# Optimization experiments

Hardware: AMD Instinct MI355X
Metric: run time of the kernel (lower is better)

## Reference

```python
import jax, jax.numpy as jnp
import numpy as np

GROUPS = 32
EPS = 1e-5


def group_norm(x, gamma, beta):
    # x: [B, C, H, W]; normalize over (C//G, H, W) within each of G groups
    B, C, H, W = x.shape
    xg = x.reshape(B, GROUPS, C // GROUPS, H, W)
    mean = xg.mean(axis=(2, 3, 4), keepdims=True)
    var = xg.var(axis=(2, 3, 4), keepdims=True)
    xg = (xg - mean) * jax.lax.rsqrt(var + EPS)
    x = xg.reshape(B, C, H, W)
    return x * gamma[None, :, None, None] + beta[None, :, None, None]


def conv1x1(x, W, b):
    # 1x1 conv == pointwise linear over channels. x: [B,C,H,W], W: [Cout,Cin]
    return jnp.einsum('oc,bchw->bohw', W, x) + b[None, :, None, None]


def setup_inputs() -> dict:
    key = jax.random.key(0)
    ks = jax.random.split(key, 6)
    B, C, H, W = 16, 512, 32, 32
    scale = 1.0 / np.sqrt(C)  # ~kaiming-ish init for 1x1 convs
    return {
        'x': jax.random.normal(ks[0], (B, C, H, W), jnp.float32),
        'gn_gamma': jnp.ones((C,), jnp.float32),
        'gn_beta': jnp.zeros((C,), jnp.float32),
        'Wq': jax.random.normal(ks[1], (C, C), jnp.float32) * scale,
        'bq': jnp.zeros((C,), jnp.float32),
        'Wk': jax.random.normal(ks[2], (C, C), jnp.float32) * scale,
        'bk': jnp.zeros((C,), jnp.float32),
        'Wv': jax.random.normal(ks[3], (C, C), jnp.float32) * scale,
        'bv': jnp.zeros((C,), jnp.float32),
        'Wp': jax.random.normal(ks[4], (C, C), jnp.float32) * scale,
        'bp': jnp.zeros((C,), jnp.float32),
    }


def reference(x, gn_gamma, gn_beta, Wq, bq, Wk, bk, Wv, bv, Wp, bp):
    B, C, H, W = x.shape
    h = group_norm(x, gn_gamma, gn_beta)
    q = conv1x1(h, Wq, bq).reshape(B, C, H * W)  # [B,C,T]
    k = conv1x1(h, Wk, bk).reshape(B, C, H * W)
    v = conv1x1(h, Wv, bv).reshape(B, C, H * W)
    # scores [B, T(query), S(key)] = q^T k, scaled by C^{-1/2}
    w = jnp.einsum('bct,bcs->bts', q, k) * (C ** -0.5)
    w = jax.nn.softmax(w, axis=-1)
    h = jnp.einsum('bts,bcs->bct', w, v).reshape(B, C, H, W)
    h = conv1x1(h, Wp, bp)
    return x + h
```

## Files before the change

### kernel.cpp

```cpp
#include <hip/hip_runtime.h>

typedef unsigned short u16;
typedef __bf16 bf16x8 __attribute__((ext_vector_type(8)));
typedef float f32x4 __attribute__((ext_vector_type(4)));

__device__ __forceinline__ u16 f2bf(float f) {
    unsigned u = __builtin_bit_cast(unsigned, f);
    u += 0x7fffu + ((u >> 16) & 1u);
    return (u16)(u >> 16);
}

#define GLDS16(g, l) __builtin_amdgcn_global_load_lds( \
    (const __attribute__((address_space(1))) void*)(g), \
    (__attribute__((address_space(3))) void*)(l), 16, 0, 0)

#define QK_SCALE 0.044194173824159216f

__global__ __launch_bounds__(256) void convert_kernel(
    const float* __restrict__ Wq, const float* __restrict__ Wk,
    const float* __restrict__ Wv, const float* __restrict__ Wp,
    const float* __restrict__ bq, const float* __restrict__ bk,
    const float* __restrict__ bv,
    u16* __restrict__ Wqkv, u16* __restrict__ Wpb, float* __restrict__ bqkv,
    float* __restrict__ rsum)
{
    int idx = blockIdx.x * 256 + threadIdx.x;
    if (idx < 786432) {
        int which = idx >> 18;
        int off   = idx & 262143;
        if (which == 0)
            Wqkv[idx] = f2bf(Wq[off] * QK_SCALE);
        else
            Wqkv[idx] = f2bf(((which == 1) ? Wk : Wv)[off]);
    } else {
        int off = idx - 786432;
        Wpb[off] = f2bf(Wp[off]);
    }
    if (idx < 1536) {
        float bvv = (idx < 512) ? bq[idx] * QK_SCALE
                  : (idx < 1024) ? bk[idx & 511] : bv[idx & 511];
        bqkv[idx] = bvv;
    }
    if (idx < 16384) rsum[idx] = 0.f;
}

__global__ __launch_bounds__(256) void gn_stats(
    const float* __restrict__ x, float2* __restrict__ stats)
{
    const int g = blockIdx.x, b = blockIdx.y, tid = threadIdx.x;
    const float* xg = x + ((size_t)b * 512 + (size_t)g * 16) * 1024;

    float s = 0.f, s2 = 0.f;
    const float4* x4 = (const float4*)xg;
    #pragma unroll 4
    for (int i = tid; i < 4096; i += 256) {
        float4 v = x4[i];
        s  += v.x + v.y + v.z + v.w;
        s2 += v.x * v.x + v.y * v.y + v.z * v.z + v.w * v.w;
    }
    #pragma unroll
    for (int off = 32; off; off >>= 1) {
        s  += __shfl_down(s, off);
        s2 += __shfl_down(s2, off);
    }
    __shared__ float rs[4], rs2[4];
    const int w = tid >> 6;
    if ((tid & 63) == 0) { rs[w] = s; rs2[w] = s2; }
    __syncthreads();
    if (tid == 0) {
        float S  = rs[0] + rs[1] + rs[2] + rs[3];
        float S2 = rs2[0] + rs2[1] + rs2[2] + rs2[3];
        float mean = S * (1.f / 16384.f);
        float var  = S2 * (1.f / 16384.f) - mean * mean;
        stats[b * 32 + g] = make_float2(mean, rsqrtf(var + 1e-5f));
    }
}

__global__ __launch_bounds__(256) void gn_apply(
    const float* __restrict__ x, const float* __restrict__ gamma,
    const float* __restrict__ beta, const float2* __restrict__ stats,
    u16* __restrict__ ht)
{
    const int tc = blockIdx.x, b = blockIdx.y, tid = threadIdx.x;
    const int t0 = tc * 32;

    __shared__ float2 st[32];
    __shared__ float ga[512], be[512];
    __shared__ __align__(16) u16 tile[512 * 32];

    if (tid < 32) st[tid] = stats[b * 32 + tid];
    for (int c = tid; c < 512; c += 256) { ga[c] = gamma[c]; be[c] = beta[c]; }
    __syncthreads();

    #pragma unroll
    for (int pass = 0; pass < 16; pass++) {
        const int c = pass * 32 + (tid >> 3);
        const int f = tid & 7;
        float4 v = *(const float4*)(x + ((size_t)(b * 512 + c)) * 1024 + t0 + f * 4);
        float2 s = st[c >> 4];
        float sc = s.y * ga[c];
        float sh = be[c] - s.x * sc;
        ushort4 hv = {f2bf(v.x * sc + sh), f2bf(v.y * sc + sh),
                      f2bf(v.z * sc + sh), f2bf(v.w * sc + sh)};
        const int slot = f ^ (c & 7) ^ ((c >> 3) & 7);
        *(ushort4*)(tile + c * 32 + slot * 4) = hv;
    }
    __syncthreads();

    #pragma unroll
    for (int p = 0; p < 8; p++) {
        const int t = p * 4 + (tid >> 6);
        const int l = tid & 63;
        u16 tmp[8];
        #pragma unroll
        for (int e = 0; e < 8; e++) {
            const int c = l * 8 + e;
            const int slot = (t >> 2) ^ (c & 7) ^ ((c >> 3) & 7);
            tmp[e] = tile[c * 32 + slot * 4 + (t & 3)];
        }
        *(uint4*)(ht + ((size_t)b * 1024 + t0 + t) * 512 + l * 8) = *(uint4*)tmp;
    }
}

template <int MODE>
__global__ __launch_bounds__(512, 2) void gemm_nt(
    const u16* __restrict__ A, const u16* __restrict__ B,
    size_t strideA, size_t strideB, int lda, int ldb, int K,
    u16* __restrict__ o0, u16* __restrict__ o1, u16* __restrict__ o2,
    float* __restrict__ fo, const float* __restrict__ bias,
    const float* __restrict__ xres)
{
    __shared__ __align__(16) u16 smem[73728];
    u16* As = smem;
    u16* Bs = smem + 49152;

    const int tid  = threadIdx.x;
    const int lane = tid & 63;
    const int wave = tid >> 6;
    const int wm   = (wave & 3) * 64;
    const int wn   = (wave >> 2) * 64;

    const int gx = gridDim.x, gy = gridDim.y;
    int f = blockIdx.x + gx * (blockIdx.y + gy * blockIdx.z);
    const int nwg = gx * gy * (int)gridDim.z;
    f = (f & 7) * (nwg >> 3) + (f >> 3);
    const int bx  = f % gx;
    const int byz = f / gx;
    const int by  = byz % gy;
    const int b   = byz / gy;

    const u16* Ab = A + (size_t)b * strideA + (size_t)by * 256 * lda;
    const u16* Bb = B + (size_t)b * strideB + (size_t)bx * 128 * ldb;

    const int srow = tid >> 3;
    const int sc   = tid & 7;
    const int scg  = sc ^ (srow & 7);

    const u16* aSrc[4]; int aDst[4];
    #pragma unroll
    for (int u = 0; u < 4; u++) {
        aSrc[u] = Ab + (size_t)(u * 64 + srow) * lda + scg * 8;
        aDst[u] = (u * 64 + srow) * 64 + sc * 8;
    }
    const u16* bSrc[2]; int bDst[2];
    #pragma unroll
    for (int u = 0; u < 2; u++) {
        bSrc[u] = Bb + (size_t)(u * 64 + srow) * ldb + scg * 8;
        bDst[u] = (u * 64 + srow) * 64 + sc * 8;
    }

    const int l15 = lane & 15, lh = lane >> 4, rx = lane & 7;
    int aOff[4][2], bOff[4][2];
    #pragma unroll
    for (int i = 0; i < 4; i++)
        #pragma unroll
        for (int ks = 0; ks < 2; ks++) {
            const int slot = ((ks << 2) + lh) ^ rx;
            aOff[i][ks] = (wm + i * 16 + l15) * 64 + slot * 8;
            bOff[i][ks] = (wn + i * 16 + l15) * 64 + slot * 8;
        }

    f32x4 acc[4][4] = {};
    const int NT = K >> 6;

    #pragma unroll
    for (int u = 0; u < 4; u++) GLDS16(aSrc[u], As + aDst[u]);
    #pragma unroll
    for (int u = 0; u < 2; u++) GLDS16(bSrc[u], Bs + bDst[u]);
    #pragma unroll
    for (int u = 0; u < 4; u++) GLDS16(aSrc[u] + 64, As + 16384 + aDst[u]);
    #pragma unroll
    for (int u = 0; u < 2; u++) GLDS16(bSrc[u] + 64, Bs + 8192 + bDst[u]);

    int cbuf = 0, sbuf = 2;
    for (int t = 0; t < NT; ++t) {
        if (t == NT - 1) asm volatile("s_waitcnt vmcnt(0)" ::: "memory");
        else             asm volatile("s_waitcnt vmcnt(6)" ::: "memory");
        __builtin_amdgcn_s_barrier();

        const u16* Ac = As + cbuf * 16384;
        const u16* Bc = Bs + cbuf * 8192;
        u16* Asb = As + sbuf * 16384;
        u16* Bsb = Bs + sbuf * 8192;
        const int ko = (t + 2) * 64;
        const bool pf = (t + 2 < NT);

        if (pf) {
            GLDS16(aSrc[0] + ko, Asb + aDst[0]);
            GLDS16(aSrc[1] + ko, Asb + aDst[1]);
            GLDS16(bSrc[0] + ko, Bsb + bDst[0]);
        }
        {
            bf16x8 af[4], bfr[4];
            #pragma unroll
            for (int i = 0; i < 4; i++) {
                af[i]  = *(const bf16x8*)(Ac + aOff[i][0]);
                bfr[i] = *(const bf16x8*)(Bc + bOff[i][0]);
            }
            __builtin_amdgcn_s_setprio(1);
            #pragma unroll
            for (int mi = 0; mi < 4; mi++)
                #pragma unroll
                for (int nj = 0; nj < 4; nj++)
                    acc[mi][nj] = __builtin_amdgcn_mfma_f32_16x16x32_bf16(
                        af[mi], bfr[nj], acc[mi][nj], 0, 0, 0);
            __builtin_amdgcn_s_setprio(0);
        }
        if (pf) {
            GLDS16(aSrc[2] + ko, Asb + aDst[2]);
            GLDS16(aSrc[3] + ko, Asb + aDst[3]);
            GLDS16(bSrc[1] + ko, Bsb + bDst[1]);
        }
        {
            bf16x8 af[4], bfr[4];
            #pragma unroll
            for (int i = 0; i < 4; i++) {
                af[i]  = *(const bf16x8*)(Ac + aOff[i][1]);
                bfr[i] = *(const bf16x8*)(Bc + bOff[i][1]);
            }
            __builtin_amdgcn_s_setprio(1);
            #pragma unroll
            for (int mi = 0; mi < 4; mi++)
                #pragma unroll
                for (int nj = 0; nj < 4; nj++)
                    acc[mi][nj] = __builtin_amdgcn_mfma_f32_16x16x32_bf16(
                        af[mi], bfr[nj], acc[mi][nj], 0, 0, 0);
            __builtin_amdgcn_s_setprio(0);
        }

        cbuf = (cbuf == 2) ? 0 : cbuf + 1;
        sbuf = (sbuf == 2) ? 0 : sbuf + 1;
    }

    const int N0 = bx * 128;
    const int M0 = by * 256;

    if (MODE == 0 && N0 < 1024) {
        u16* dst = (N0 < 512) ? o0 : o1;
        const int nn0 = N0 & 511;
        #pragma unroll
        for (int nj = 0; nj < 4; nj++) {
            const int n = wn + nj * 16 + l15;
            const float bv = bias[N0 + n];
            #pragma unroll
            for (int mi = 0; mi < 4; mi++) {
                const int mq = M0 + wm + mi * 16 + lh * 4;
                const size_t base = ((size_t)b * 1024 + mq) * 512 + nn0 + n;
                dst[base]        = f2bf(acc[mi][nj][0] + bv);
                dst[base + 512]  = f2bf(acc[mi][nj][1] + bv);
                dst[base + 1024] = f2bf(acc[mi][nj][2] + bv);
                dst[base + 1536] = f2bf(acc[mi][nj][3] + bv);
            }
        }
    } else if (MODE != 3) {
        __syncthreads();
        float rinv_[4];
        if (MODE == 2) {
            #pragma unroll
            for (int nj = 0; nj < 4; nj++)
                rinv_[nj] = 1.0f / xres[(size_t)b * 1024 + N0 + wn + nj * 16 + l15];
        }
        #pragma unroll
        for (int mi = 0; mi < 4; mi++) {
            const int mq = wm + mi * 16 + lh * 4;
            #pragma unroll
            for (int nj = 0; nj < 4; nj++) {
                const int n = wn + nj * 16 + l15;
                float a0 = acc[mi][nj][0], a1 = acc[mi][nj][1];
                float a2 = acc[mi][nj][2], a3 = acc[mi][nj][3];
                if (MODE == 0) {
                    const float bv = bias[N0 + n];
                    a0 += bv; a1 += bv; a2 += bv; a3 += bv;
                }
                if (MODE == 1) {
                    a0 = __expf(a0); a1 = __expf(a1);
                    a2 = __expf(a2); a3 = __expf(a3);
                }
                if (MODE == 2) {
                    a0 *= rinv_[nj]; a1 *= rinv_[nj];
                    a2 *= rinv_[nj]; a3 *= rinv_[nj];
                }
                ushort4 hv = {f2bf(a0), f2bf(a1), f2bf(a2), f2bf(a3)};
                *(ushort4*)((char*)smem + n * 512 +
                            (((mq >> 3) ^ (n & 31)) << 4) + ((mq >> 2) & 1) * 8) = hv;
            }
        }
        __syncthreads();
        #pragma unroll
        for (int p = 0; p < 8; p++) {
            const int n  = p * 16 + (tid >> 5);
            const int gi = tid & 31;
            uint4 v4 = *(const uint4*)((char*)smem + n * 512 +
                                       ((gi ^ (n & 31)) << 4));
            u16* dst;
            if (MODE == 0)      dst = o2 + ((size_t)b * 512 + (N0 - 1024) + n) * 1024 + M0;
            else if (MODE == 1) dst = o0 + ((size_t)b * 1024 + N0 + n) * 1024 + M0;
            else                dst = o0 + ((size_t)b * 1024 + N0 + n) * 512 + M0;
            *(uint4*)(dst + gi * 8) = v4;
            if (MODE == 1) {
                unsigned wd_[4] = {v4.x, v4.y, v4.z, v4.w};
                float rsm = 0.f;
                #pragma unroll
                for (int q = 0; q < 4; q++)
                    rsm += __builtin_bit_cast(float, wd_[q] << 16)
                         + __builtin_bit_cast(float, wd_[q] & 0xffff0000u);
                #pragma unroll
                for (int off = 1; off < 32; off <<= 1)
                    rsm += __shfl_xor(rsm, off);
                if (gi == 0)
                    atomicAdd(fo + ((size_t)b * 1024 + N0 + n), rsm);
            }
        }
    } else {
        __syncthreads();
        float* smf = (float*)smem;
        #pragma unroll
        for (int mi = 0; mi < 4; mi++) {
            const int mq = wm + mi * 16 + lh * 4;
            #pragma unroll
            for (int nj = 0; nj < 4; nj++) {
                const int n = wn + nj * 16 + l15;
                float4 v4 = {acc[mi][nj][0], acc[mi][nj][1],
                             acc[mi][nj][2], acc[mi][nj][3]};
                *(float4*)((char*)smf + n * 1024 +
                           (((mq >> 2) ^ (n & 63)) << 4)) = v4;
            }
        }
        __syncthreads();
        #pragma unroll
        for (int p = 0; p < 16; p++) {
            const int n  = p * 8 + (tid >> 6);
            const int gi = tid & 63;
            float4 v4 = *(const float4*)((char*)smf + n * 1024 +
                                         ((gi ^ (n & 63)) << 4));
            const size_t off = ((size_t)b * 512 + N0 + n) * 1024 + M0 + gi * 4;
            const float bv = bias[N0 + n];
            const float4 xv = *(const float4*)(xres + off);
            float4 ov = {v4.x + bv + xv.x, v4.y + bv + xv.y,
                         v4.z + bv + xv.z, v4.w + bv + xv.w};
            *(float4*)(fo + off) = ov;
        }
    }
}

extern "C" void kernel_launch(void* const* d_in, const int* in_sizes, int n_in,
                              void* d_out, int out_size, void* d_ws, size_t ws_size,
                              hipStream_t stream)
{
    const float* x     = (const float*)d_in[0];
    const float* gamma = (const float*)d_in[1];
    const float* beta  = (const float*)d_in[2];
    const float* Wq    = (const float*)d_in[3];
    const float* bq    = (const float*)d_in[4];
    const float* Wk    = (const float*)d_in[5];
    const float* bk    = (const float*)d_in[6];
    const float* Wv    = (const float*)d_in[7];
    const float* bv    = (const float*)d_in[8];
    const float* Wp    = (const float*)d_in[9];
    const float* bp    = (const float*)d_in[10];

    char* ws = (char*)d_ws;
    u16*   Wqkv   = (u16*)(ws + 0);
    u16*   Wpb    = (u16*)(ws + 1572864);
    float* bqkv   = (float*)(ws + 2097152);
    u16*   ht     = (u16*)(ws + 2105344);
    u16*   kt     = (u16*)(ws + 18882560);
    u16*   vv     = (u16*)(ws + 35659776);
    u16*   scores = (u16*)(ws + 52436992);
    u16*   qt  = (u16*)d_out;
    float2* stats = (float2*)((char*)d_out + 16777216);
    float* rsum   = (float*)((char*)d_out + 16781312);
    u16*   h2  = ht;
    float* out = (float*)d_out;

    convert_kernel<<<4096, 256, 0, stream>>>(Wq, Wk, Wv, Wp, bq, bk, bv,
                                             Wqkv, Wpb, bqkv, rsum);
    gn_stats<<<dim3(32, 16), 256, 0, stream>>>(x, stats);
    gn_apply<<<dim3(32, 16), 256, 0, stream>>>(x, gamma, beta, stats, ht);

    gemm_nt<0><<<dim3(12, 4, 16), 512, 0, stream>>>(
        ht, Wqkv, 524288, 0, 512, 512, 512,
        qt, kt, vv, nullptr, bqkv, nullptr);

    gemm_nt<1><<<dim3(8, 4, 16), 512, 0, stream>>>(
        kt, qt, 524288, 524288, 512, 512, 512,
        scores, nullptr, nullptr, rsum, nullptr, nullptr);

    gemm_nt<2><<<dim3(8, 2, 16), 512, 0, stream>>>(
        vv, scores, 524288, 1048576, 1024, 1024, 1024,
        h2, nullptr, nullptr, nullptr, nullptr, rsum);

    gemm_nt<3><<<dim3(4, 4, 16), 512, 0, stream>>>(
        h2, Wpb, 524288, 0, 512, 512, 512,
        nullptr, nullptr, nullptr, out, bp, x);
}
```

Baseline: 222.1 us.

## Fuse QK^T, exp and PV into a single flash-style attention kernel

```diff
diff --git a/kernel.cpp b/kernel.cpp
--- a/kernel.cpp
+++ b/kernel.cpp
@@ -8,6 +8,9 @@
     unsigned u = __builtin_bit_cast(unsigned, f);
     u += 0x7fffu + ((u >> 16) & 1u);
     return (u16)(u >> 16);
+}
+__device__ __forceinline__ float bf2f(u16 h) {
+    return __builtin_bit_cast(float, (unsigned)h << 16);
 }
 
 #define GLDS16(g, l) __builtin_amdgcn_global_load_lds( \
@@ -21,8 +24,7 @@
     const float* __restrict__ Wv, const float* __restrict__ Wp,
     const float* __restrict__ bq, const float* __restrict__ bk,
     const float* __restrict__ bv,
-    u16* __restrict__ Wqkv, u16* __restrict__ Wpb, float* __restrict__ bqkv,
-    float* __restrict__ rsum)
+    u16* __restrict__ Wqkv, u16* __restrict__ Wpb, float* __restrict__ bqkv)
 {
     int idx = blockIdx.x * 256 + threadIdx.x;
     if (idx < 786432) {
@@ -41,7 +43,6 @@
                   : (idx < 1024) ? bk[idx & 511] : bv[idx & 511];
         bqkv[idx] = bvv;
     }
-    if (idx < 16384) rsum[idx] = 0.f;
 }
 
 __global__ __launch_bounds__(256) void gn_stats(
@@ -122,6 +123,149 @@
     }
 }
 
+__global__ __launch_bounds__(512, 2) void flash64(
+    const u16* __restrict__ q,
+    const u16* __restrict__ k,
+    const u16* __restrict__ v,
+    u16* __restrict__ o)
+{
+    __shared__ __align__(16) u16 smem[66688];
+
+    const int tid  = threadIdx.x;
+    const int lane = tid & 63;
+    const int wave = tid >> 6;
+    const int l15  = lane & 15;
+    const int lh   = lane >> 4;
+    const int rx   = lane & 7;
+
+    const int flat  = blockIdx.x;
+    const int b     = ((flat & 7) << 1) | (flat >> 7);
+    const int qtile = (flat >> 3) & 15;
+    const int t0    = qtile * 64;
+
+    const u16* Qg = q + ((size_t)b * 1024 + t0) * 512;
+    const u16* Kg = k + (size_t)b * 524288;
+    const u16* Vg = v + (size_t)b * 524288;
+    u16*       Og = o + ((size_t)b * 1024 + t0) * 512;
+
+    #pragma unroll
+    for (int u = 0; u < 8; u++) {
+        const int r0 = wave + 8 * u;
+        GLDS16(Qg + r0 * 512 + (lane ^ (r0 & 7)) * 8,
+               smem + r0 * 512 + lane * 8);
+    }
+    asm volatile("s_waitcnt vmcnt(0)" ::: "memory");
+    __syncthreads();
+
+    f32x4 oacc[4][4] = {};
+    float rs_[16] = {};
+
+    for (int st = 0; st < 4; st++) {
+        u16* Pc = smem + 32768 + (st & 1) * 16384;
+        const u16* Kst = Kg + (size_t)(st * 256) * 512;
+        f32x4 sacc[4][2] = {};
+
+        #pragma unroll
+        for (int i = 0; i < 16; i++) {
+            bf16x8 af[4], bfr[2];
+            #pragma unroll
+            for (int mi = 0; mi < 4; mi++)
+                af[mi] = *(const bf16x8*)(smem + (mi * 16 + l15) * 512 +
+                                          (((i * 4 + lh) ^ rx) << 3));
+            #pragma unroll
+            for (int nj = 0; nj < 2; nj++)
+                bfr[nj] = *(const bf16x8*)(Kst +
+                          (size_t)(wave * 32 + nj * 16 + l15) * 512 + i * 32 + lh * 8);
+            __builtin_amdgcn_s_setprio(1);
+            #pragma unroll
+            for (int mi = 0; mi < 4; mi++)
+                #pragma unroll
+                for (int nj = 0; nj < 2; nj++)
+                    sacc[mi][nj] = __builtin_amdgcn_mfma_f32_16x16x32_bf16(
+                        af[mi], bfr[nj], sacc[mi][nj], 0, 0, 0);
+            __builtin_amdgcn_s_setprio(0);
+        }
+
+        #pragma unroll
+        for (int mi = 0; mi < 4; mi++) {
+            #pragma unroll
+            for (int nj = 0; nj < 2; nj++) {
+                #pragma unroll
+                for (int r = 0; r < 4; r++) {
+                    float e = __expf(sacc[mi][nj][r]);
+                    u16 h = f2bf(e);
+                    rs_[mi * 4 + r] += bf2f(h);
+                    const int tr = mi * 16 + lh * 4 + r;
+                    const int s  = wave * 32 + nj * 16 + l15;
+                    Pc[tr * 256 + (((s >> 3) ^ (tr & 7)) << 3) + (s & 7)] = h;
+                }
+            }
+        }
+        asm volatile("s_waitcnt lgkmcnt(0)" ::: "memory");
+        __builtin_amdgcn_s_barrier();
+
+        const u16* Vst = Vg + st * 256;
+        #pragma unroll
+        for (int j = 0; j < 8; j++) {
+            bf16x8 pa[4], vb[4];
+            #pragma unroll
+            for (int mi = 0; mi < 4; mi++)
+                pa[mi] = *(const bf16x8*)(Pc + (mi * 16 + l15) * 256 +
+                                          (((j * 4 + lh) ^ rx) << 3));
+            #pragma unroll
+            for (int nj = 0; nj < 4; nj++)
+                vb[nj] = *(const bf16x8*)(Vst +
+                         (size_t)(wave * 64 + nj * 16 + l15) * 1024 + j * 32 + lh * 8);
+            __builtin_amdgcn_s_setprio(1);
+            #pragma unroll
+            for (int mi = 0; mi < 4; mi++)
+                #pragma unroll
+                for (int nj = 0; nj < 4; nj++)
+                    oacc[mi][nj] = __builtin_amdgcn_mfma_f32_16x16x32_bf16(
+                        pa[mi], vb[nj], oacc[mi][nj], 0, 0, 0);
+            __builtin_amdgcn_s_setprio(0);
+        }
+    }
+
+    float* rl = (float*)(smem + 65536);
+    #pragma unroll
+    for (int i = 0; i < 16; i++) {
+        rs_[i] += __shfl_xor(rs_[i], 1);
+        rs_[i] += __shfl_xor(rs_[i], 2);
+        rs_[i] += __shfl_xor(rs_[i], 4);
+        rs_[i] += __shfl_xor(rs_[i], 8);
+    }
+    if (l15 == 0) {
+        #pragma unroll
+        for (int mi = 0; mi < 4; mi++)
+            #pragma unroll
+            for (int r = 0; r < 4; r++)
+                rl[wave * 64 + mi * 16 + lh * 4 + r] = rs_[mi * 4 + r];
+    }
+    __syncthreads();
+    if (tid < 64) {
+        float tot = 0.f;
+        #pragma unroll
+        for (int w = 0; w < 8; w++) tot += rl[w * 64 + tid];
+        rl[512 + tid] = 1.0f / tot;
+    }
+    __syncthreads();
+    float ri_[16];
+    #pragma unroll
+    for (int mi = 0; mi < 4; mi++)
+        #pragma unroll
+        for (int r = 0; r < 4; r++)
+            ri_[mi * 4 + r] = rl[512 + mi * 16 + lh * 4 + r];
+    #pragma unroll
+    for (int mi = 0; mi < 4; mi++)
+        #pragma unroll
+        for (int nj = 0; nj < 4; nj++)
+            #pragma unroll
+            for (int r = 0; r < 4; r++)
+                Og[(size_t)(mi * 16 + lh * 4 + r) * 512 + wave * 64 + nj * 16 + l15]
+                    = f2bf(oacc[mi][nj][r] * ri_[mi * 4 + r]);
+}
+
 template <int MODE>
 __global__ __launch_bounds__(512, 2) void gemm_nt(
     const u16* __restrict__ A, const u16* __restrict__ B,
@@ -272,35 +416,17 @@
                 dst[base + 1536] = f2bf(acc[mi][nj][3] + bv);
             }
         }
-    } else if (MODE != 3) {
+    } else if (MODE == 0) {
         __syncthreads();
-        float rinv_[4];
-        if (MODE == 2) {
-            #pragma unroll
-            for (int nj = 0; nj < 4; nj++)
-                rinv_[nj] = 1.0f / xres[(size_t)b * 1024 + N0 + wn + nj * 16 + l15];
-        }
         #pragma unroll
         for (int mi = 0; mi < 4; mi++) {
             const int mq = wm + mi * 16 + lh * 4;
             #pragma unroll
             for (int nj = 0; nj < 4; nj++) {
                 const int n = wn + nj * 16 + l15;
-                float a0 = acc[mi][nj][0], a1 = acc[mi][nj][1];
-                float a2 = acc[mi][nj][2], a3 = acc[mi][nj][3];
-                if (MODE == 0) {
-                    const float bv = bias[N0 + n];
-                    a0 += bv; a1 += bv; a2 += bv; a3 += bv;
-                }
-                if (MODE == 1) {
-                    a0 = __expf(a0); a1 = __expf(a1);
-                    a2 = __expf(a2); a3 = __expf(a3);
-                }
-                if (MODE == 2) {
-                    a0 *= rinv_[nj]; a1 *= rinv_[nj];
-                    a2 *= rinv_[nj]; a3 *= rinv_[nj];
-                }
-                ushort4 hv = {f2bf(a0), f2bf(a1), f2bf(a2), f2bf(a3)};
+                const float bv = bias[N0 + n];
+                ushort4 hv = {f2bf(acc[mi][nj][0] + bv), f2bf(acc[mi][nj][1] + bv),
+                              f2bf(acc[mi][nj][2] + bv), f2bf(acc[mi][nj][3] + bv)};
                 *(ushort4*)((char*)smem + n * 512 +
                             (((mq >> 3) ^ (n & 31)) << 4) + ((mq >> 2) & 1) * 8) = hv;
             }
@@ -312,24 +438,8 @@
             const int gi = tid & 31;
             uint4 v4 = *(const uint4*)((char*)smem + n * 512 +
                                        ((gi ^ (n & 31)) << 4));
-            u16* dst;
-            if (MODE == 0)      dst = o2 + ((size_t)b * 512 + (N0 - 1024) + n) * 1024 + M0;
-            else if (MODE == 1) dst = o0 + ((size_t)b * 1024 + N0 + n) * 1024 + M0;
-            else                dst = o0 + ((size_t)b * 1024 + N0 + n) * 512 + M0;
+            u16* dst = o2 + ((size_t)b * 512 + (N0 - 1024) + n) * 1024 + M0;
             *(uint4*)(dst + gi * 8) = v4;
-            if (MODE == 1) {
-                unsigned wd_[4] = {v4.x, v4.y, v4.z, v4.w};
-                float rsm = 0.f;
-                #pragma unroll
-                for (int q = 0; q < 4; q++)
-                    rsm += __builtin_bit_cast(float, wd_[q] << 16)
-                         + __builtin_bit_cast(float, wd_[q] & 0xffff0000u);
-                #pragma unroll
-                for (int off = 1; off < 32; off <<= 1)
-                    rsm += __shfl_xor(rsm, off);
-                if (gi == 0)
-                    atomicAdd(fo + ((size_t)b * 1024 + N0 + n), rsm);
-            }
         }
     } else {
         __syncthreads();
@@ -386,15 +496,13 @@
     u16*   ht     = (u16*)(ws + 2105344);
     u16*   kt     = (u16*)(ws + 18882560);
     u16*   vv     = (u16*)(ws + 35659776);
-    u16*   scores = (u16*)(ws + 52436992);
     u16*   qt  = (u16*)d_out;
     float2* stats = (float2*)((char*)d_out + 16777216);
-    float* rsum   = (float*)((char*)d_out + 16781312);
     u16*   h2  = ht;
     float* out = (float*)d_out;
 
     convert_kernel<<<4096, 256, 0, stream>>>(Wq, Wk, Wv, Wp, bq, bk, bv,
-                                             Wqkv, Wpb, bqkv, rsum);
+                                             Wqkv, Wpb, bqkv);
     gn_stats<<<dim3(32, 16), 256, 0, stream>>>(x, stats);
     gn_apply<<<dim3(32, 16), 256, 0, stream>>>(x, gamma, beta, stats, ht);
 
@@ -402,13 +510,7 @@
         ht, Wqkv, 524288, 0, 512, 512, 512,
         qt, kt, vv, nullptr, bqkv, nullptr);
 
-    gemm_nt<1><<<dim3(8, 4, 16), 512, 0, stream>>>(
-        kt, qt, 524288, 524288, 512, 512, 512,
-        scores, nullptr, nullptr, rsum, nullptr, nullptr);
-
-    gemm_nt<2><<<dim3(8, 2, 16), 512, 0, stream>>>(
-        vv, scores, 524288, 1048576, 1024, 1024, 1024,
-        h2, nullptr, nullptr, nullptr, nullptr, rsum);
+    flash64<<<256, 512, 0, stream>>>(qt, kt, vv, h2);
 
     gemm_nt<3><<<dim3(4, 4, 16), 512, 0, stream>>>(
         h2, Wpb, 524288, 0, 512, 512, 512,
```

Result: slower. 236.2 us (+6.3%).

## Add 128x128-tile GEMM with 32x32 MFMA for score, PV and projection stages

Applied to the files above, without the earlier changes.

```diff
diff --git a/kernel.cpp b/kernel.cpp
--- a/kernel.cpp
+++ b/kernel.cpp
@@ -3,11 +3,15 @@
 typedef unsigned short u16;
 typedef __bf16 bf16x8 __attribute__((ext_vector_type(8)));
 typedef float f32x4 __attribute__((ext_vector_type(4)));
+typedef float f32x16 __attribute__((ext_vector_type(16)));
 
 __device__ __forceinline__ u16 f2bf(float f) {
     unsigned u = __builtin_bit_cast(unsigned, f);
     u += 0x7fffu + ((u >> 16) & 1u);
     return (u16)(u >> 16);
+}
+__device__ __forceinline__ float bf2f(u16 h) {
+    return __builtin_bit_cast(float, (unsigned)h << 16);
 }
 
 #define GLDS16(g, l) __builtin_amdgcn_global_load_lds( \
@@ -123,12 +127,11 @@
 }
 
 template <int MODE>
-__global__ __launch_bounds__(512, 2) void gemm_nt(
+__global__ __launch_bounds__(512, 2) void gemm_big(
     const u16* __restrict__ A, const u16* __restrict__ B,
     size_t strideA, size_t strideB, int lda, int ldb, int K,
     u16* __restrict__ o0, u16* __restrict__ o1, u16* __restrict__ o2,
-    float* __restrict__ fo, const float* __restrict__ bias,
-    const float* __restrict__ xres)
+    const float* __restrict__ bias)
 {
     __shared__ __align__(16) u16 smem[73728];
     u16* As = smem;
@@ -255,7 +258,7 @@
     const int N0 = bx * 128;
     const int M0 = by * 256;
 
-    if (MODE == 0 && N0 < 1024) {
+    if (N0 < 1024) {
         u16* dst = (N0 < 512) ? o0 : o1;
         const int nn0 = N0 & 511;
         #pragma unroll
@@ -272,35 +275,17 @@
                 dst[base + 1536] = f2bf(acc[mi][nj][3] + bv);
             }
         }
-    } else if (MODE != 3) {
+    } else {
         __syncthreads();
-        float rinv_[4];
-        if (MODE == 2) {
-            #pragma unroll
-            for (int nj = 0; nj < 4; nj++)
-                rinv_[nj] = 1.0f / xres[(size_t)b * 1024 + N0 + wn + nj * 16 + l15];
-        }
         #pragma unroll
         for (int mi = 0; mi < 4; mi++) {
             const int mq = wm + mi * 16 + lh * 4;
             #pragma unroll
             for (int nj = 0; nj < 4; nj++) {
                 const int n = wn + nj * 16 + l15;
-                float a0 = acc[mi][nj][0], a1 = acc[mi][nj][1];
-                float a2 = acc[mi][nj][2], a3 = acc[mi][nj][3];
-                if (MODE == 0) {
-                    const float bv = bias[N0 + n];
-                    a0 += bv; a1 += bv; a2 += bv; a3 += bv;
-                }
-                if (MODE == 1) {
-                    a0 = __expf(a0); a1 = __expf(a1);
-                    a2 = __expf(a2); a3 = __expf(a3);
-                }
-                if (MODE == 2) {
-                    a0 *= rinv_[nj]; a1 *= rinv_[nj];
-                    a2 *= rinv_[nj]; a3 *= rinv_[nj];
-                }
-                ushort4 hv = {f2bf(a0), f2bf(a1), f2bf(a2), f2bf(a3)};
+                const float bv = bias[N0 + n];
+                ushort4 hv = {f2bf(acc[mi][nj][0] + bv), f2bf(acc[mi][nj][1] + bv),
+                              f2bf(acc[mi][nj][2] + bv), f2bf(acc[mi][nj][3] + bv)};
                 *(ushort4*)((char*)smem + n * 512 +
                             (((mq >> 3) ^ (n & 31)) << 4) + ((mq >> 2) & 1) * 8) = hv;
             }
@@ -312,53 +297,168 @@
             const int gi = tid & 31;
             uint4 v4 = *(const uint4*)((char*)smem + n * 512 +
                                        ((gi ^ (n & 31)) << 4));
+            u16* dst = o2 + ((size_t)b * 512 + (N0 - 1024) + n) * 1024 + M0;
+            *(uint4*)(dst + gi * 8) = v4;
+        }
+    }
+}
+
+template <int MODE>
+__global__ __launch_bounds__(256, 4) void gemm128(
+    const u16* __restrict__ A, const u16* __restrict__ B,
+    size_t strideA, size_t strideB, int lda, int ldb, int K,
+    u16* __restrict__ o0,
+    float* __restrict__ fo, const float* __restrict__ bias,
+    const float* __restrict__ xres)
+{
+    __shared__ __align__(16) u16 sm[16384];
+    u16* As = sm;
+    u16* Bs = sm + 8192;
+
+    const int tid   = threadIdx.x;
+    const int lane  = tid & 63;
+    const int wave  = tid >> 6;
+    const int wm    = (wave >> 1) * 64;
+    const int wn    = (wave & 1) * 64;
+    const int l31   = lane & 31;
+    const int khalf = lane >> 5;
+
+    const int gx = gridDim.x, gy = gridDim.y;
+    int f = blockIdx.x + gx * (blockIdx.y + gy * blockIdx.z);
+    const int nwg = gx * gy * (int)gridDim.z;
+    f = (f & 7) * (nwg >> 3) + (f >> 3);
+    const int bx  = f % gx;
+    const int byz = f / gx;
+    const int by  = byz % gy;
+    const int b   = byz / gy;
+
+    const u16* Ab = A + (size_t)b * strideA + (size_t)by * 128 * lda;
+    const u16* Bb = B + (size_t)b * strideB + (size_t)bx * 128 * ldb;
+
+    const int srow = lane >> 3;
+    const int sc   = lane & 7;
+    const int scg  = sc ^ srow;
+
+    f32x16 acc[2][2] = {};
+
+    for (int k0 = 0; k0 < K; k0 += 64) {
+        __syncthreads();
+        #pragma unroll
+        for (int s = 0; s < 4; s++) {
+            const int r = wave * 32 + s * 8 + srow;
+            GLDS16(Ab + (size_t)r * lda + k0 + scg * 8, As + r * 64 + sc * 8);
+            GLDS16(Bb + (size_t)r * ldb + k0 + scg * 8, Bs + r * 64 + sc * 8);
+        }
+        __syncthreads();
+
+        #pragma unroll
+        for (int ks = 0; ks < 4; ks++) {
+            const int cidx = ks * 2 + khalf;
+            const int slot = (cidx ^ (lane & 7)) * 8;
+            bf16x8 af[2], bfr[2];
+            #pragma unroll
+            for (int i = 0; i < 2; i++)
+                af[i] = *(const bf16x8*)(As + (wm + i * 32 + l31) * 64 + slot);
+            #pragma unroll
+            for (int j = 0; j < 2; j++)
+                bfr[j] = *(const bf16x8*)(Bs + (wn + j * 32 + l31) * 64 + slot);
+            #pragma unroll
+            for (int i = 0; i < 2; i++)
+                #pragma unroll
+                for (int j = 0; j < 2; j++)
+                    acc[i][j] = __builtin_amdgcn_mfma_f32_32x32x16_bf16(
+                        af[i], bfr[j], acc[i][j], 0, 0, 0);
+        }
+    }
+
+    const int N0 = bx * 128;
+    const int M0 = by * 128;
+
+    if (MODE != 3) {
+        __syncthreads();
+        float rinv_[2];
+        if (MODE == 2) {
+            #pragma unroll
+            for (int j = 0; j < 2; j++)
+                rinv_[j] = 1.0f / xres[(size_t)b * 1024 + N0 + wn + j * 32 + l31];
+        }
+        #pragma unroll
+        for (int i = 0; i < 2; i++) {
+            #pragma unroll
+            for (int j = 0; j < 2; j++) {
+                const int n = wn + j * 32 + l31;
+                #pragma unroll
+                for (int g = 0; g < 4; g++) {
+                    const int m = wm + 4 * khalf + i * 32 + 8 * g;
+                    float a0 = acc[i][j][4 * g],     a1 = acc[i][j][4 * g + 1];
+                    float a2 = acc[i][j][4 * g + 2], a3 = acc[i][j][4 * g + 3];
+                    if (MODE == 1) {
+                        a0 = __expf(a0); a1 = __expf(a1);
+                        a2 = __expf(a2); a3 = __expf(a3);
+                    }
+                    if (MODE == 2) {
+                        a0 *= rinv_[j]; a1 *= rinv_[j];
+                        a2 *= rinv_[j]; a3 *= rinv_[j];
+                    }
+                    ushort4 hv = {f2bf(a0), f2bf(a1), f2bf(a2), f2bf(a3)};
+                    *(ushort4*)(sm + n * 128 + (((m >> 3) ^ (n & 15)) << 3) + (m & 7)) = hv;
+                }
+            }
+        }
+        __syncthreads();
+        #pragma unroll
+        for (int p = 0; p < 8; p++) {
+            const int n  = p * 16 + (tid >> 4);
+            const int gi = tid & 15;
+            uint4 v = *(const uint4*)(sm + n * 128 + ((gi ^ (n & 15)) << 3));
             u16* dst;
-            if (MODE == 0)      dst = o2 + ((size_t)b * 512 + (N0 - 1024) + n) * 1024 + M0;
-            else if (MODE == 1) dst = o0 + ((size_t)b * 1024 + N0 + n) * 1024 + M0;
-            else                dst = o0 + ((size_t)b * 1024 + N0 + n) * 512 + M0;
-            *(uint4*)(dst + gi * 8) = v4;
+            if (MODE == 1) dst = o0 + ((size_t)b * 1024 + N0 + n) * 1024 + M0;
+            else           dst = o0 + ((size_t)b * 1024 + N0 + n) * 512 + M0;
+            *(uint4*)(dst + gi * 8) = v;
             if (MODE == 1) {
-                unsigned wd_[4] = {v4.x, v4.y, v4.z, v4.w};
+                unsigned wd_[4] = {v.x, v.y, v.z, v.w};
                 float rsm = 0.f;
                 #pragma unroll
                 for (int q = 0; q < 4; q++)
                     rsm += __builtin_bit_cast(float, wd_[q] << 16)
                          + __builtin_bit_cast(float, wd_[q] & 0xffff0000u);
                 #pragma unroll
-                for (int off = 1; off < 32; off <<= 1)
+                for (int off = 1; off < 16; off <<= 1)
                     rsm += __shfl_xor(rsm, off);
                 if (gi == 0)
                     atomicAdd(fo + ((size_t)b * 1024 + N0 + n), rsm);
             }
         }
     } else {
-        __syncthreads();
-        float* smf = (float*)smem;
-        #pragma unroll
-        for (int mi = 0; mi < 4; mi++) {
-            const int mq = wm + mi * 16 + lh * 4;
-            #pragma unroll
-            for (int nj = 0; nj < 4; nj++) {
-                const int n = wn + nj * 16 + l15;
-                float4 v4 = {acc[mi][nj][0], acc[mi][nj][1],
-                             acc[mi][nj][2], acc[mi][nj][3]};
-                *(float4*)((char*)smf + n * 1024 +
-                           (((mq >> 2) ^ (n & 63)) << 4)) = v4;
-            }
-        }
-        __syncthreads();
-        #pragma unroll
-        for (int p = 0; p < 16; p++) {
-            const int n  = p * 8 + (tid >> 6);
-            const int gi = tid & 63;
-            float4 v4 = *(const float4*)((char*)smf + n * 1024 +
-                                         ((gi ^ (n & 63)) << 4));
-            const size_t off = ((size_t)b * 512 + N0 + n) * 1024 + M0 + gi * 4;
-            const float bv = bias[N0 + n];
-            const float4 xv = *(const float4*)(xres + off);
-            float4 ov = {v4.x + bv + xv.x, v4.y + bv + xv.y,
-                         v4.z + bv + xv.z, v4.w + bv + xv.w};
-            *(float4*)(fo + off) = ov;
+        float* smf = (float*)sm;
+        #pragma unroll
+        for (int i = 0; i < 2; i++) {
+            __syncthreads();
+            #pragma unroll
+            for (int j = 0; j < 2; j++) {
+                const int n = wn + j * 32 + l31;
+                #pragma unroll
+                for (int g = 0; g < 4; g++) {
+                    const int mIdx = 4 * khalf + 8 * g + ((wm >> 6) << 5);
+                    float4 v4 = {acc[i][j][4 * g],     acc[i][j][4 * g + 1],
+                                 acc[i][j][4 * g + 2], acc[i][j][4 * g + 3]};
+                    *(float4*)(smf + n * 64 + (((mIdx >> 2) ^ (n & 15)) << 2)) = v4;
+                }
+            }
+            __syncthreads();
+            #pragma unroll
+            for (int p = 0; p < 8; p++) {
+                const int n  = p * 16 + (tid >> 4);
+                const int gi = tid & 15;
+                float4 v = *(const float4*)(smf + n * 64 + ((gi ^ (n & 15)) << 2));
+                const int m = (gi & 7) * 4 + ((gi >> 3) << 6) + 32 * i;
+                const size_t off = ((size_t)b * 512 + N0 + n) * 1024 + M0 + m;
+                const float bv = bias[N0 + n];
+                const float4 xv = *(const float4*)(xres + off);
+                float4 ov = {v.x + bv + xv.x, v.y + bv + xv.y,
+                             v.z + bv + xv.z, v.w + bv + xv.w};
+                *(float4*)(fo + off) = ov;
+            }
         }
     }
 }
@@ -398,19 +498,19 @@
     gn_stats<<<dim3(32, 16), 256, 0, stream>>>(x, stats);
     gn_apply<<<dim3(32, 16), 256, 0, stream>>>(x, gamma, beta, stats, ht);
 
-    gemm_nt<0><<<dim3(12, 4, 16), 512, 0, stream>>>(
+    gemm_big<0><<<dim3(12, 4, 16), 512, 0, stream>>>(
         ht, Wqkv, 524288, 0, 512, 512, 512,
-        qt, kt, vv, nullptr, bqkv, nullptr);
-
-    gemm_nt<1><<<dim3(8, 4, 16), 512, 0, stream>>>(
+        qt, kt, vv, bqkv);
+
+    gemm128<1><<<dim3(8, 8, 16), 256, 0, stream>>>(
         kt, qt, 524288, 524288, 512, 512, 512,
-        scores, nullptr, nullptr, rsum, nullptr, nullptr);
-
-    gemm_nt<2><<<dim3(8, 2, 16), 512, 0, stream>>>(
+        scores, rsum, nullptr, nullptr);
+
+    gemm128<2><<<dim3(8, 4, 16), 256, 0, stream>>>(
         vv, scores, 524288, 1048576, 1024, 1024, 1024,
-        h2, nullptr, nullptr, nullptr, nullptr, rsum);
-
-    gemm_nt<3><<<dim3(4, 4, 16), 512, 0, stream>>>(
+        h2, nullptr, nullptr, rsum);
+
+    gemm128<3><<<dim3(4, 8, 16), 256, 0, stream>>>(
         h2, Wpb, 524288, 0, 512, 512, 512,
-        nullptr, nullptr, nullptr, out, bp, x);
-}
+        nullptr, out, bp, x);
+}
```

New measurement: 227.1 us. +2.2%, slower.
